# Performance work log

Hardware: AMD Instinct MI355X
Metric: run time of the kernel (lower is better)

## Reference

```python
import jax, jax.numpy as jnp
import numpy as np

B, L, E, Fm, Y, K = 16, 2500, 100, 50, 8921, 10
PAD = K // 2  # floor(kernel_size/2) = 5; even kernel -> output length L+1, as in torch


def setup_inputs() -> dict:
    key = jax.random.key(0)
    ks = jax.random.split(key, 6)
    x = jax.random.normal(ks[0], (B, L, E), dtype=jnp.float32)
    target = (jax.random.uniform(ks[1], (B, Y)) < 0.01).astype(jnp.float32)
    conv_w = jax.random.normal(ks[2], (Fm, E, K), dtype=jnp.float32) * 0.05  # (out, in, k)
    conv_b = jnp.zeros((Fm,), jnp.float32)
    U_w = jax.random.normal(ks[3], (Y, Fm), dtype=jnp.float32) * 0.05
    final_w = jax.random.normal(ks[4], (Y, Fm), dtype=jnp.float32) * 0.05
    final_b = jnp.zeros((Y,), jnp.float32)
    return dict(x=x, target=target, conv_w=conv_w, conv_b=conv_b,
                U_w=U_w, final_w=final_w, final_b=final_b)


def reference(x, target, conv_w, conv_b, U_w, final_w, final_b):
    # dropout is identity in eval mode
    xc = jnp.transpose(x, (0, 2, 1))  # (B, E, L)
    h = jax.lax.conv_general_dilated(
        xc, conv_w, window_strides=(1,), padding=[(PAD, PAD)],
        dimension_numbers=('NCH', 'OIH', 'NCH'))  # (B, Fm, L+1)
    h = jnp.tanh(jnp.transpose(h + conv_b[None, :, None], (0, 2, 1)))  # (B, Lp, Fm)
    # label-wise attention: U.weight @ h^T -> (B, Y, Lp)
    scores = jnp.einsum('yf,blf->byl', U_w, h)
    alpha = jax.nn.softmax(scores, axis=2)          # (B, Y, Lp) -- dominant memory traffic
    m = jnp.einsum('byl,blf->byf', alpha, h)        # (B, Y, Fm)
    logits = jnp.sum(final_w[None, :, :] * m, axis=2) + final_b  # (B, Y)
    proba = jax.nn.log_softmax(logits, axis=1)
    # binary_cross_entropy_with_logits, mean reduction (numerically stable form)
    loss = jnp.mean(jnp.maximum(logits, 0) - logits * target
                    + jnp.log1p(jnp.exp(-jnp.abs(logits))))
    return proba, loss, alpha
```

## Files before the change

kernel.cpp:

```cpp
#include <hip/hip_runtime.h>
#include <math.h>

#define Bn 16
#define Ln 2500
#define En 100
#define FM 50
#define Yn 8921
#define KS 10
#define LP 2501
#define NT 40
#define TILE_BYTES 19456
#define TILE_SHORTS 9728
#define HT_OFF 5120
#define CH_FULL 19
#define CH_A 10
#define NW 8
#define YB 128
#define NYB 70

typedef __attribute__((ext_vector_type(8))) short short8;
typedef __attribute__((ext_vector_type(4))) float f32x4;

union S8 { short8 v; long l2[2]; short s[8]; };

__device__ __forceinline__ short f2bf(float f){
  unsigned u = __float_as_uint(f);
  unsigned r = (u + 0x7fffu + ((u >> 16) & 1u)) >> 16;
  return (short)r;
}

__device__ __forceinline__ void g2l16(const void* g, void* l){
  __builtin_amdgcn_global_load_lds(
      (const __attribute__((address_space(1))) unsigned int*)g,
      (__attribute__((address_space(3))) unsigned int*)l, 16, 0, 0);
}

__device__ __forceinline__ void stage_chunks(const char* __restrict__ gbase,
                                             char* lbase, int wave, int lane,
                                             int nch, int nw){
  for (int chunk = wave; chunk < nch; chunk += nw)
    g2l16(gbase + chunk * 1024 + lane * 16, lbase + chunk * 1024 + lane * 16);
}

__global__ void k0_wt(const float* __restrict__ cw, float* __restrict__ WT){
  int i = blockIdx.x * 256 + threadIdx.x;
  if (i < 64000){
    int f = i & 63, ek = i >> 6;
    WT[i] = (f < FM) ? cw[f * 1000 + ek] : 0.f;
  }
}

__global__ __launch_bounds__(256) void k1_conv(
    const float* __restrict__ x, const float* __restrict__ WT,
    const float* __restrict__ conv_b, short* __restrict__ Hp)
{
  int t = blockIdx.x, b = blockIdx.y, tid = threadIdx.x;
  __shared__ float x_s[100 * 76];
  __shared__ short h_t[64 * 69];

  int r0 = 64 * t - 5;
  for (int d = tid; d < 7300; d += 256){
    int row = d / 100, e = d - row * 100;
    int gr = r0 + row;
    float v = (gr >= 0 && gr < Ln) ? x[((size_t)b * Ln + gr) * 100 + e] : 0.f;
    x_s[e * 76 + row] = v;
  }
  __syncthreads();

  int f = tid & 63, lsub = tid >> 6;
  float acc[16];
#pragma unroll
  for (int j = 0; j < 16; j++) acc[j] = 0.f;

  for (int e = 0; e < 100; e++){
    float xv[25];
    const float* xr = x_s + e * 76 + lsub * 16;
#pragma unroll
    for (int i = 0; i < 6; i++){
      f32x4 q = *(const f32x4*)(xr + 4 * i);
      xv[4*i+0] = q[0]; xv[4*i+1] = q[1]; xv[4*i+2] = q[2]; xv[4*i+3] = q[3];
    }
    xv[24] = xr[24];
#pragma unroll
    for (int k = 0; k < KS; k++){
      float wv = WT[(e * 10 + k) * 64 + f];
#pragma unroll
      for (int j = 0; j < 16; j++) acc[j] += wv * xv[j + k];
    }
  }

  float bias = (f < FM) ? conv_b[f] : 0.f;
  size_t tbS = (size_t)(b * NT + t) * TILE_SHORTS;
#pragma unroll
  for (int j = 0; j < 16; j++){
    int l = lsub * 16 + j;
    int lgl = 64 * t + l;
    float hv = (lgl < LP && f < FM) ? tanhf(acc[j] + bias) : 0.f;
    short hb = f2bf(hv);
    Hp[tbS + (size_t)(f >> 4) * 1280 + (size_t)l * 20 + (f & 15)] = hb;
    h_t[l * 69 + f] = hb;
  }
  __syncthreads();
  int lane = tid & 63, wave = tid >> 6;
#pragma unroll
  for (int i = 0; i < 16; i++){
    int fo = wave + 4 * i;
    Hp[tbS + HT_OFF + (size_t)fo * 72 + lane] = h_t[lane * 69 + fo];
  }
}

__device__ __forceinline__ void scores_tile(const short* __restrict__ h_s,
                                            const S8 bu[2], int c, int g, f32x4 d[4])
{
#pragma unroll
  for (int ms = 0; ms < 4; ms++){
    f32x4 acc = {0.f, 0.f, 0.f, 0.f};
#pragma unroll
    for (int kf = 0; kf < 2; kf++){
      const short* pa = h_s + (2 * kf) * 1280 + (c + 16 * ms) * 20 + 4 * g;
      S8 a;
      a.l2[0] = *(const long*)pa;
      a.l2[1] = *(const long*)(pa + 1280);
      acc = __builtin_amdgcn_mfma_f32_16x16x32_bf16(a.v, bu[kf].v, acc, 0, 0, 0);
    }
    d[ms] = acc;
  }
}

__device__ __forceinline__ void load_bu(const float* __restrict__ U_w,
                                        int ywave, int c, int g, S8 bu[2]){
  int yv = ywave + c;
#pragma unroll
  for (int kf = 0; kf < 2; kf++)
#pragma unroll
    for (int i = 0; i < 8; i++){
      int fidx = 4 * g + (i & 3) + 16 * (i >> 2) + 32 * kf;
      float v = (yv < Yn && fidx < FM) ? U_w[yv * FM + fidx] : 0.f;
      bu[kf].s[i] = f2bf(v);
    }
}

__global__ __launch_bounds__(512, 4) void k2a_sum(
    const short* __restrict__ Hp, const float* __restrict__ U_w,
    float* __restrict__ invS_out)
{
  int id = blockIdx.x;
  int xcd = id & 7, rr = id >> 3;
  int b   = xcd + ((rr >= NYB) ? 8 : 0);
  int y0  = ((rr >= NYB) ? rr - NYB : rr) * YB;

  int tid = threadIdx.x;
  int lane = tid & 63, wave = tid >> 6;
  int c = lane & 15, g = lane >> 4;
  int ywave = y0 + wave * 16;

  __shared__ __align__(16) short buf[2][5120];

  S8 bu[2];
  load_bu(U_w, ywave, c, g, bu);

  const char* blob = (const char*)Hp + (size_t)b * NT * TILE_BYTES;

  float S = 0.f;
  int cur = 0;
  stage_chunks(blob, (char*)buf[0], wave, lane, CH_A, NW);
  for (int t = 0; t < NT; t++){
    __syncthreads();
    if (t + 1 < NT)
      stage_chunks(blob + (size_t)(t + 1) * TILE_BYTES, (char*)buf[cur ^ 1], wave, lane, CH_A, NW);
    f32x4 d[4];
    scores_tile(buf[cur], bu, c, g, d);
    if (t < NT - 1){
#pragma unroll
      for (int ms = 0; ms < 4; ms++)
#pragma unroll
        for (int q = 0; q < 4; q++) S += __expf(d[ms][q]);
    } else {
#pragma unroll
      for (int ms = 0; ms < 4; ms++)
#pragma unroll
        for (int q = 0; q < 4; q++){
          int l = 64 * t + 16 * ms + 4 * g + q;
          if (l < LP) S += __expf(d[ms][q]);
        }
    }
    cur ^= 1;
  }
  S += __shfl_xor(S, 16);
  S += __shfl_xor(S, 32);
  if (lane < 16){
    int yv = ywave + lane;
    if (yv < Yn) invS_out[b * Yn + yv] = 1.f / S;
  }
}

__global__ __launch_bounds__(512, 4) void k2b_alpha(
    const short* __restrict__ Hp,
    const float* __restrict__ U_w, const float* __restrict__ final_w,
    const float* __restrict__ final_b, const float* __restrict__ invS_arr,
    float* __restrict__ logits, float* __restrict__ alpha_out,
    float* __restrict__ dump)
{
  int id = blockIdx.x;
  int xcd = id & 7, rr = id >> 3;
  int b   = xcd + ((rr >= NYB) ? 8 : 0);
  int y0  = ((rr >= NYB) ? rr - NYB : rr) * YB;

  int tid = threadIdx.x;
  int lane = tid & 63, wave = tid >> 6;
  int c = lane & 15, g = lane >> 4;
  int ywave = y0 + wave * 16;

  __shared__ __align__(16) short buf[2][TILE_SHORTS];
  __shared__ float awf[NW * 1024];

  S8 bu[2];
  load_bu(U_w, ywave, c, g, bu);

  float invS = 0.f;
  { int yv = ywave + c; if (yv < Yn) invS = invS_arr[b * Yn + yv]; }

  int Kf = (17 + 29 * b + 5 * ywave) & 31;
  int fc = (Kf + 5 * c) & 31;

  f32x4 m2[4];
#pragma unroll
  for (int fs = 0; fs < 4; fs++) m2[fs] = (f32x4){0.f, 0.f, 0.f, 0.f};

  const char* blob = (const char*)Hp + (size_t)b * NT * TILE_BYTES;
  float* aw = awf + wave * 1024;
  float* dumpf = dump + (size_t)id * 64;

  int cur = 0;
  stage_chunks(blob, (char*)buf[0], wave, lane, CH_FULL, NW);
  for (int t = 0; t < NT; t++){
    if (t == 0) asm volatile("s_waitcnt vmcnt(0) lgkmcnt(0)" ::: "memory");
    else        asm volatile("s_waitcnt vmcnt(16) lgkmcnt(0)" ::: "memory");
    __builtin_amdgcn_s_barrier();
    if (t + 1 < NT)
      stage_chunks(blob + (size_t)(t + 1) * TILE_BYTES, (char*)buf[cur ^ 1], wave, lane, CH_FULL, NW);
    __builtin_amdgcn_sched_barrier(0);

    const short* h_s  = buf[cur];
    const short* ht_s = buf[cur] + HT_OFF;
    f32x4 d[4];
    scores_tile(h_s, bu, c, g, d);
    float a[16];
    if (t < NT - 1){
#pragma unroll
      for (int ms = 0; ms < 4; ms++)
#pragma unroll
        for (int q = 0; q < 4; q++) a[ms * 4 + q] = __expf(d[ms][q]) * invS;
    } else {
#pragma unroll
      for (int ms = 0; ms < 4; ms++)
#pragma unroll
        for (int q = 0; q < 4; q++){
          int l = 64 * t + 16 * ms + 4 * g + q;
          a[ms * 4 + q] = (l < LP) ? __expf(d[ms][q]) * invS : 0.f;
        }
    }

#pragma unroll
    for (int kl = 0; kl < 2; kl++){
      S8 a2;
#pragma unroll
      for (int i = 0; i < 8; i++)
        a2.s[i] = f2bf(a[(2 * kl + (i >> 2)) * 4 + (i & 3)]);
#pragma unroll
      for (int fs = 0; fs < 4; fs++){
        const short* pb = ht_s + (16 * fs + c) * 72 + 4 * g + 32 * kl;
        S8 b2;
        b2.l2[0] = *(const long*)pb;
        b2.l2[1] = *(const long*)(pb + 16);
        m2[fs] = __builtin_amdgcn_mfma_f32_16x16x32_bf16(a2.v, b2.v, m2[fs], 0, 0, 0);
      }
    }

#pragma unroll
    for (int hs = 0; hs < 2; hs++){
#pragma unroll
      for (int mh = 0; mh < 2; mh++)
#pragma unroll
        for (int q = 0; q < 4; q++)
          aw[c * 64 + fc + 16 * mh + 4 * g + q] = a[(2 * hs + mh) * 4 + q];
#pragma unroll
      for (int i = 0; i < 8; i++){
        int jj  = 2 * i + (lane >> 5);
        int k32 = lane & 31;
        int fj  = (Kf + 5 * jj) & 31;
        int gcol = 64 * t + 32 * hs - fj + k32;
        float v = aw[jj * 64 + k32];
        int yj = ywave + jj;
        bool ok = (gcol >= 0) & (gcol < LP) & (yj < Yn);
        float* dst = ok ? (alpha_out + (size_t)(b * Yn + yj) * LP + gcol)
                        : (dumpf + lane);
        __builtin_nontemporal_store(v, dst);
      }
#pragma unroll
      for (int i = 0; i < 8; i++){
        int jj  = 2 * i + (lane >> 5);
        int k32 = lane & 31;
        int fj  = (Kf + 5 * jj) & 31;
        if (k32 < fj) aw[jj * 64 + k32] = aw[jj * 64 + 32 + k32];
      }
    }
    cur ^= 1;
  }

  float part[4];
#pragma unroll
  for (int q = 0; q < 4; q++){
    int yy = ywave + 4 * g + q;
    float p = 0.f;
    if (yy < Yn){
#pragma unroll
      for (int fs = 0; fs < 4; fs++){
        int fcol = fs * 16 + c;
        if (fcol < FM) p += m2[fs][q] * final_w[yy * FM + fcol];
      }
    }
#pragma unroll
    for (int off = 1; off <= 8; off <<= 1) p += __shfl_xor(p, off);
    part[q] = p;
  }
  if (c == 0){
#pragma unroll
    for (int q = 0; q < 4; q++){
      int yy = ywave + 4 * g + q;
      if (yy < Yn) logits[(size_t)b * Yn + yy] = part[q] + final_b[yy];
    }
  }
}

__global__ __launch_bounds__(256) void k3_lsm(
    const float* __restrict__ logits, const float* __restrict__ target,
    float* __restrict__ proba, float* __restrict__ lossp)
{
  int b = blockIdx.x, tid = threadIdx.x;
  int lane = tid & 63, wave = tid >> 6;
  __shared__ float red[4];
  const float* lg = logits + (size_t)b * Yn;
  const float* tg = target + (size_t)b * Yn;

  float m = -INFINITY;
  for (int y = tid; y < Yn; y += 256) m = fmaxf(m, lg[y]);
#pragma unroll
  for (int off = 1; off <= 32; off <<= 1) m = fmaxf(m, __shfl_xor(m, off));
  if (lane == 0) red[wave] = m;
  __syncthreads();
  m = fmaxf(fmaxf(red[0], red[1]), fmaxf(red[2], red[3]));
  __syncthreads();

  float s = 0.f;
  for (int y = tid; y < Yn; y += 256) s += __expf(lg[y] - m);
#pragma unroll
  for (int off = 1; off <= 32; off <<= 1) s += __shfl_xor(s, off);
  if (lane == 0) red[wave] = s;
  __syncthreads();
  s = red[0] + red[1] + red[2] + red[3];
  __syncthreads();
  float lse = m + logf(s);

  float ls = 0.f;
  for (int y = tid; y < Yn; y += 256){
    float xx = lg[y];
    proba[(size_t)b * Yn + y] = xx - lse;
    ls += fmaxf(xx, 0.f) - xx * tg[y] + log1pf(__expf(-fabsf(xx)));
  }
#pragma unroll
  for (int off = 1; off <= 32; off <<= 1) ls += __shfl_xor(ls, off);
  if (lane == 0) red[wave] = ls;
  __syncthreads();
  if (tid == 0) lossp[b] = red[0] + red[1] + red[2] + red[3];
}

__global__ void k4_loss(const float* __restrict__ lossp, float* __restrict__ out){
  if (threadIdx.x == 0){
    float s = 0.f;
    for (int i = 0; i < Bn; i++) s += lossp[i];
    out[142736] = s / 142736.f;
  }
}

extern "C" void kernel_launch(void* const* d_in, const int* in_sizes, int n_in,
                              void* d_out, int out_size, void* d_ws, size_t ws_size,
                              hipStream_t stream)
{
  const float* x       = (const float*)d_in[0];
  const float* target  = (const float*)d_in[1];
  const float* conv_w  = (const float*)d_in[2];
  const float* conv_b  = (const float*)d_in[3];
  const float* U_w     = (const float*)d_in[4];
  const float* final_w = (const float*)d_in[5];
  const float* final_b = (const float*)d_in[6];
  float* out = (float*)d_out;

  char* ws = (char*)d_ws;
  short* Hp     = (short*)(ws);
  float* WT     = (float*)(ws + 12451840);
  float* logits = (float*)(ws + 12707840);
  float* lossp  = (float*)(ws + 13278784);
  float* invS   = (float*)(ws + 13278848);
  float* dump   = (float*)(ws + 13849792);

  float* proba     = out;
  float* alpha_out = out + 142737;

  k0_wt<<<dim3(250), dim3(256), 0, stream>>>(conv_w, WT);
  k1_conv<<<dim3(NT, Bn), dim3(256), 0, stream>>>(x, WT, conv_b, Hp);
  k2a_sum<<<dim3(8 * 2 * NYB), dim3(512), 0, stream>>>(Hp, U_w, invS);
  k2b_alpha<<<dim3(8 * 2 * NYB), dim3(512), 0, stream>>>(Hp, U_w, final_w, final_b,
                                                         invS, logits, alpha_out, dump);
  k3_lsm<<<dim3(Bn), dim3(256), 0, stream>>>(logits, target, proba, lossp);
  k4_loss<<<dim3(1), dim3(64), 0, stream>>>(lossp, out);
}
```

Measured before the change: 600.9 us.

## Fuse softmax-sum and alpha kernels into one pass, remap conv blocks per XCD

```diff
diff --git a/kernel.cpp b/kernel.cpp
--- a/kernel.cpp
+++ b/kernel.cpp
@@ -54,7 +54,11 @@
     const float* __restrict__ x, const float* __restrict__ WT,
     const float* __restrict__ conv_b, short* __restrict__ Hp)
 {
-  int t = blockIdx.x, b = blockIdx.y, tid = threadIdx.x;
+  int id = blockIdx.x;
+  int xcd = id & 7, rr = id >> 3;
+  int b   = xcd + ((rr >= NT) ? 8 : 0);
+  int t   = (rr >= NT) ? rr - NT : rr;
+  int tid = threadIdx.x;
   __shared__ float x_s[100 * 76];
   __shared__ short h_t[64 * 69];
 
@@ -140,9 +144,12 @@
     }
 }
 
-__global__ __launch_bounds__(512, 4) void k2a_sum(
-    const short* __restrict__ Hp, const float* __restrict__ U_w,
-    float* __restrict__ invS_out)
+__global__ __launch_bounds__(512, 4) void k2_fused(
+    const short* __restrict__ Hp,
+    const float* __restrict__ U_w, const float* __restrict__ final_w,
+    const float* __restrict__ final_b,
+    float* __restrict__ logits, float* __restrict__ alpha_out,
+    float* __restrict__ dump)
 {
   int id = blockIdx.x;
   int xcd = id & 7, rr = id >> 3;
@@ -154,7 +161,8 @@
   int c = lane & 15, g = lane >> 4;
   int ywave = y0 + wave * 16;
 
-  __shared__ __align__(16) short buf[2][5120];
+  __shared__ __align__(16) short buf[2][TILE_SHORTS];
+  __shared__ float awf[NW * 1024];
 
   S8 bu[2];
   load_bu(U_w, ywave, c, g, bu);
@@ -162,63 +170,36 @@
   const char* blob = (const char*)Hp + (size_t)b * NT * TILE_BYTES;
 
   float S = 0.f;
-  int cur = 0;
-  stage_chunks(blob, (char*)buf[0], wave, lane, CH_A, NW);
-  for (int t = 0; t < NT; t++){
-    __syncthreads();
-    if (t + 1 < NT)
-      stage_chunks(blob + (size_t)(t + 1) * TILE_BYTES, (char*)buf[cur ^ 1], wave, lane, CH_A, NW);
-    f32x4 d[4];
-    scores_tile(buf[cur], bu, c, g, d);
-    if (t < NT - 1){
-#pragma unroll
-      for (int ms = 0; ms < 4; ms++)
-#pragma unroll
-        for (int q = 0; q < 4; q++) S += __expf(d[ms][q]);
-    } else {
-#pragma unroll
-      for (int ms = 0; ms < 4; ms++)
-#pragma unroll
-        for (int q = 0; q < 4; q++){
-          int l = 64 * t + 16 * ms + 4 * g + q;
-          if (l < LP) S += __expf(d[ms][q]);
-        }
-    }
-    cur ^= 1;
+  {
+    int cur = 0;
+    stage_chunks(blob, (char*)buf[0], wave, lane, CH_A, NW);
+    for (int t = 0; t < NT; t++){
+      __syncthreads();
+      if (t + 1 < NT)
+        stage_chunks(blob + (size_t)(t + 1) * TILE_BYTES, (char*)buf[cur ^ 1], wave, lane, CH_A, NW);
+      f32x4 d[4];
+      scores_tile(buf[cur], bu, c, g, d);
+      if (t < NT - 1){
+#pragma unroll
+        for (int ms = 0; ms < 4; ms++)
+#pragma unroll
+          for (int q = 0; q < 4; q++) S += __expf(d[ms][q]);
+      } else {
+#pragma unroll
+        for (int ms = 0; ms < 4; ms++)
+#pragma unroll
+          for (int q = 0; q < 4; q++){
+            int l = 64 * t + 16 * ms + 4 * g + q;
+            if (l < LP) S += __expf(d[ms][q]);
+          }
+      }
+      cur ^= 1;
+    }
   }
   S += __shfl_xor(S, 16);
   S += __shfl_xor(S, 32);
-  if (lane < 16){
-    int yv = ywave + lane;
-    if (yv < Yn) invS_out[b * Yn + yv] = 1.f / S;
-  }
-}
-
-__global__ __launch_bounds__(512, 4) void k2b_alpha(
-    const short* __restrict__ Hp,
-    const float* __restrict__ U_w, const float* __restrict__ final_w,
-    const float* __restrict__ final_b, const float* __restrict__ invS_arr,
-    float* __restrict__ logits, float* __restrict__ alpha_out,
-    float* __restrict__ dump)
-{
-  int id = blockIdx.x;
-  int xcd = id & 7, rr = id >> 3;
-  int b   = xcd + ((rr >= NYB) ? 8 : 0);
-  int y0  = ((rr >= NYB) ? rr - NYB : rr) * YB;
-
-  int tid = threadIdx.x;
-  int lane = tid & 63, wave = tid >> 6;
-  int c = lane & 15, g = lane >> 4;
-  int ywave = y0 + wave * 16;
-
-  __shared__ __align__(16) short buf[2][TILE_SHORTS];
-  __shared__ float awf[NW * 1024];
-
-  S8 bu[2];
-  load_bu(U_w, ywave, c, g, bu);
-
-  float invS = 0.f;
-  { int yv = ywave + c; if (yv < Yn) invS = invS_arr[b * Yn + yv]; }
+  float invS = 1.f / S;
+  __syncthreads();
 
   int Kf = (17 + 29 * b + 5 * ywave) & 31;
   int fc = (Kf + 5 * c) & 31;
@@ -227,7 +208,6 @@
 #pragma unroll
   for (int fs = 0; fs < 4; fs++) m2[fs] = (f32x4){0.f, 0.f, 0.f, 0.f};
 
-  const char* blob = (const char*)Hp + (size_t)b * NT * TILE_BYTES;
   float* aw = awf + wave * 1024;
   float* dumpf = dump + (size_t)id * 64;
 
@@ -401,17 +381,15 @@
   float* WT     = (float*)(ws + 12451840);
   float* logits = (float*)(ws + 12707840);
   float* lossp  = (float*)(ws + 13278784);
-  float* invS   = (float*)(ws + 13278848);
-  float* dump   = (float*)(ws + 13849792);
+  float* dump   = (float*)(ws + 13278848);
 
   float* proba     = out;
   float* alpha_out = out + 142737;
 
   k0_wt<<<dim3(250), dim3(256), 0, stream>>>(conv_w, WT);
-  k1_conv<<<dim3(NT, Bn), dim3(256), 0, stream>>>(x, WT, conv_b, Hp);
-  k2a_sum<<<dim3(8 * 2 * NYB), dim3(512), 0, stream>>>(Hp, U_w, invS);
-  k2b_alpha<<<dim3(8 * 2 * NYB), dim3(512), 0, stream>>>(Hp, U_w, final_w, final_b,
-                                                         invS, logits, alpha_out, dump);
+  k1_conv<<<dim3(8 * 2 * NT), dim3(256), 0, stream>>>(x, WT, conv_b, Hp);
+  k2_fused<<<dim3(8 * 2 * NYB), dim3(512), 0, stream>>>(Hp, U_w, final_w, final_b,
+                                                        logits, alpha_out, dump);
   k3_lsm<<<dim3(Bn), dim3(256), 0, stream>>>(logits, target, proba, lossp);
   k4_loss<<<dim3(1), dim3(64), 0, stream>>>(lossp, out);
 }
```

Result: no change. 600.8 us (-0.0%).
